# Optimization experiments

Hardware: AMD Instinct MI355X
Metric: run time of the kernel (lower is better)

## Reference

```python
import jax, jax.numpy as jnp
import numpy as np
from jax import lax

B, DZ, H, U, T, V = 256, 512, 512, 16, 16, 512  # batch, latent, lstm hidden, segments, steps/segment, vocab


def setup_inputs() -> dict:
    key = jax.random.key(0)
    ks = jax.random.split(key, 32)
    w = lambda k, shape: jax.random.normal(k, shape, jnp.float32) * 0.05
    d = {
        'z': jax.random.normal(ks[0], (B, DZ), jnp.float32),
        'x': jax.random.randint(ks[1], (B, U * T), 0, V),
        # conductor init-state projection: DZ -> 4H
        'Wc': w(ks[2], (4 * H, DZ)), 'bc': jnp.zeros((4 * H,), jnp.float32),
        # conductor 2-layer LSTM (input H, hidden H)
        'cWih0': w(ks[3], (4 * H, H)), 'cWhh0': w(ks[4], (4 * H, H)),
        'cbih0': jnp.zeros((4 * H,), jnp.float32), 'cbhh0': jnp.zeros((4 * H,), jnp.float32),
        'cWih1': w(ks[5], (4 * H, H)), 'cWhh1': w(ks[6], (4 * H, H)),
        'cbih1': jnp.zeros((4 * H,), jnp.float32), 'cbhh1': jnp.zeros((4 * H,), jnp.float32),
        # decoder init-state projection: H -> 4H
        'Wd': w(ks[7], (4 * H, H)), 'bd': jnp.zeros((4 * H,), jnp.float32),
        # decoder 2-layer LSTM (layer0 input 2H, layer1 input H, hidden H)
        'dWih0': w(ks[8], (4 * H, 2 * H)), 'dWhh0': w(ks[9], (4 * H, H)),
        'dbih0': jnp.zeros((4 * H,), jnp.float32), 'dbhh0': jnp.zeros((4 * H,), jnp.float32),
        'dWih1': w(ks[10], (4 * H, H)), 'dWhh1': w(ks[11], (4 * H, H)),
        'dbih1': jnp.zeros((4 * H,), jnp.float32), 'dbhh1': jnp.zeros((4 * H,), jnp.float32),
        # token embedding and output distribution head
        'emb': w(ks[12], (V, H)),
        'Wo': w(ks[13], (V, H)), 'bo': jnp.zeros((V,), jnp.float32),
    }
    return d


def _cell(x, h, c, Wih, Whh, bih, bhh):
    # PyTorch LSTM gate order: i, f, g, o
    g = x @ Wih.T + bih + h @ Whh.T + bhh
    i, f, gg, o = jnp.split(g, 4, axis=-1)
    c = jax.nn.sigmoid(f) * c + jax.nn.sigmoid(i) * jnp.tanh(gg)
    h = jax.nn.sigmoid(o) * jnp.tanh(c)
    return h, c


def _lstm_layer(xp, h0, c0, Whh, bhh):
    # xp: [N, T, 4H] = precomputed x @ Wih.T + bih
    def step(carry, xg):
        h, c = carry
        g = xg + h @ Whh.T + bhh
        i, f, gg, o = jnp.split(g, 4, axis=-1)
        c = jax.nn.sigmoid(f) * c + jax.nn.sigmoid(i) * jnp.tanh(gg)
        h = jax.nn.sigmoid(o) * jnp.tanh(c)
        return (h, c), h
    _, ys = lax.scan(step, (h0, c0), jnp.swapaxes(xp, 0, 1))
    return jnp.swapaxes(ys, 0, 1)  # [N, T, H]


def reference(z, x, Wc, bc, cWih0, cWhh0, cbih0, cbhh0, cWih1, cWhh1, cbih1, cbhh1,
              Wd, bd, dWih0, dWhh0, dbih0, dbhh0, dWih1, dWhh1, dbih1, dbhh1,
              emb, Wo, bo):
    Bz = z.shape[0]
    # --- conductor ---
    ci = jnp.tanh(z @ Wc.T + bc)  # [B, 4H]
    h1, h2, c1, c2 = ci[:, :H], ci[:, H:2 * H], ci[:, 2 * H:3 * H], ci[:, 3 * H:]
    o0 = jnp.zeros((Bz, H), ci.dtype)

    def cstep(carry, _):
        o, h1, c1, h2, c2 = carry
        h1, c1 = _cell(o, h1, c1, cWih0, cWhh0, cbih0, cbhh0)
        h2, c2 = _cell(h1, h2, c2, cWih1, cWhh1, cbih1, cbhh1)
        return (h2, h1, c1, h2, c2), h2

    _, couts = lax.scan(cstep, (o0, h1, c1, h2, c2), None, length=U)
    cond_out = jnp.swapaxes(couts, 0, 1)  # [B, U, H]

    # --- decoder init states ---
    states = jnp.tanh(cond_out @ Wd.T + bd).reshape(Bz * U, 4 * H)
    dh1, dh2, dc1, dc2 = (states[:, :H], states[:, H:2 * H],
                          states[:, 2 * H:3 * H], states[:, 3 * H:])
    h_init = dh1 + dh2  # [BU, H]

    # --- teacher-forced decoder ---
    xt = x.reshape(Bz * U, T)
    e = emb[xt]  # [BU, T, H]
    e = jnp.concatenate([jnp.zeros((Bz * U, 1, H), e.dtype), e[:, :-1]], axis=1)
    inp = jnp.concatenate(
        [e, jnp.broadcast_to(h_init[:, None], (Bz * U, T, H))], axis=-1)  # [BU, T, 2H]

    y0 = _lstm_layer(inp @ dWih0.T + dbih0, dh1, dc1, dWhh0, dbhh0)
    y1 = _lstm_layer(y0 @ dWih1.T + dbih1, dh2, dc2, dWhh1, dbhh1)
    dist = jax.nn.softmax(y1 @ Wo.T + bo, axis=-1)  # [BU, T, V]
    return dist.reshape(Bz, U * T, V)
```

## Files before the change

kernel.cpp:

```cpp
#include <hip/hip_runtime.h>
#include <math.h>

#define AS1 __attribute__((address_space(1)))
#define AS3 __attribute__((address_space(3)))

typedef __attribute__((ext_vector_type(8))) short short8v;
typedef __attribute__((ext_vector_type(16))) float f32x16;

constexpr size_t PA4c = (size_t)4096 * 512;
constexpr size_t PABc = (size_t)256 * 512;

__device__ __forceinline__ float sigmoidf_(float x) { return 1.f / (1.f + expf(-x)); }
__device__ __forceinline__ unsigned int f2bfu(float f) {
    unsigned int u = __float_as_uint(f);
    return (u + 0x7FFF + ((u >> 16) & 1)) >> 16;
}
__device__ __forceinline__ float bf2f(unsigned int s) { return __uint_as_float(s << 16); }
__device__ __forceinline__ unsigned int pack2(float v) {
    unsigned int b0 = f2bfu(v);
    unsigned int b1 = f2bfu(v - bf2f(b0));
    return b0 | (b1 << 16);
}
__device__ __forceinline__ float unpack2(unsigned int p) { return bf2f(p & 0xffffu) + bf2f(p >> 16); }

__device__ __forceinline__ void xswz(int d, int ngx, int ngy, int& bx, int& by) {
    int nwg = ngx * ngy;
    int q = nwg >> 3, r = nwg & 7, xcd = d & 7, pos = d >> 3;
    int logical = (xcd < r ? xcd * (q + 1) : r * (q + 1) + (xcd - r) * q) + pos;
    bx = logical % ngx; by = logical / ngx;
}

__device__ __forceinline__ size_t offf(int m, int k) {
    return ((size_t)((m >> 5) * 64 + (k >> 3))) * 256 + (size_t)((m & 31) * 8 + (k & 7));
}

__device__ __forceinline__ void store2_coh(unsigned short* p, unsigned int v) {
    asm volatile("global_store_short %0, %1, off sc0 sc1" :: "v"(p), "v"(v) : "memory");
}

template<int N>
__device__ __forceinline__ void wait_vm() {
    asm volatile("s_waitcnt vmcnt(%0) lgkmcnt(0)" :: "n"(N) : "memory");
}

template<int FM, int FN, int NBUF, bool COHB>
__device__ __forceinline__ void gemm_core(
    const short* __restrict__ A1, const short* __restrict__ B1,
    const short* __restrict__ A2, const short* __restrict__ B2,
    int M, int N, int nsteps, int pairSwitch,
    int bx, int by, short* lds, f32x16 (&acc)[FM][FN])
{
    constexpr int ABLK = 4 * FM, BBLK = 2 * FN;
    constexpr int ACH = 2 * ABLK * 2, BCH = 2 * BBLK * 2;
    constexpr int CHT = ACH + BCH;
    constexpr int CPW = CHT / 8;
    constexpr int BUFSH = CHT * 512;
    const int tid = threadIdx.x, lane = tid & 63, wid = tid >> 6;
    const int wm = wid >> 1, wn = wid & 1;
    const int l31 = lane & 31, loct = lane >> 5;
    const int mblk0 = by * ABLK, nblk0 = bx * BBLK;
    const size_t planeA = (size_t)M * 512, planeB = (size_t)N * 512;

    const short* cur[CPW];
    const short* nxt[CPW];
    int ldo[CPW];
    bool isB[CPW];
    #pragma unroll
    for (int i = 0; i < CPW; ++i) {
        int c = wid * CPW + i;
        ldo[i] = c * 512;
        size_t off;
        const short *b1, *b2;
        if (c < ACH) {
            int plane = c / (ABLK * 2), rem = c % (ABLK * 2), blk = rem >> 1, piece = rem & 1;
            off = (size_t)plane * planeA + (size_t)(mblk0 + blk) * 16384 + piece * 512 + lane * 8;
            b1 = A1; b2 = A2; isB[i] = false;
        } else {
            int cb = c - ACH;
            int plane = cb / (BBLK * 2), rem = cb % (BBLK * 2), blk = rem >> 1, piece = rem & 1;
            off = (size_t)plane * planeB + (size_t)(nblk0 + blk) * 16384 + piece * 512 + lane * 8;
            b1 = B1; b2 = B2; isB[i] = true;
        }
        cur[i] = b1 + off;
        nxt[i] = b2 ? (b2 + off) : (b1 + off);
    }

    #pragma unroll
    for (int fm = 0; fm < FM; ++fm)
        #pragma unroll
        for (int fn = 0; fn < FN; ++fn)
            acc[fm][fn] = (f32x16){};

    auto STAGE = [&](int bufIdx) {
        short* db = lds + bufIdx * BUFSH;
        #pragma unroll
        for (int i = 0; i < CPW; ++i) {
            if constexpr (COHB) {
                if (isB[i])
                    __builtin_amdgcn_global_load_lds((const AS1 unsigned int*)cur[i],
                                                     (AS3 unsigned int*)(db + ldo[i]), 16, 0, 17);
                else
                    __builtin_amdgcn_global_load_lds((const AS1 unsigned int*)cur[i],
                                                     (AS3 unsigned int*)(db + ldo[i]), 16, 0, 0);
            } else {
                __builtin_amdgcn_global_load_lds((const AS1 unsigned int*)cur[i],
                                                 (AS3 unsigned int*)(db + ldo[i]), 16, 0, 0);
            }
            cur[i] += 1024;
        }
    };

    #pragma unroll
    for (int i = 0; i < NBUF - 1; ++i) STAGE(i);
    wait_vm<CPW * (NBUF - 2)>();
    __builtin_amdgcn_s_barrier();

    for (int t = 0; t < nsteps; ++t) {
        int s = t + NBUF - 1;
        if (s < nsteps) {
            if (s == pairSwitch) {
                #pragma unroll
                for (int i = 0; i < CPW; ++i) cur[i] = nxt[i];
            }
            STAGE(s % NBUF);
        }
        const short* L = lds + (t % NBUF) * BUFSH;
        #pragma unroll
        for (int ksub = 0; ksub < 2; ++ksub) {
            short8v a[FM][2], b[FN][2];
            #pragma unroll
            for (int p = 0; p < 2; ++p) {
                #pragma unroll
                for (int f = 0; f < FM; ++f)
                    a[f][p] = *(const short8v*)(L + (p * (ABLK * 2) + (wm * FM + f) * 2 + ksub) * 512
                                                  + loct * 256 + l31 * 8);
                #pragma unroll
                for (int f = 0; f < FN; ++f)
                    b[f][p] = *(const short8v*)(L + (ACH + p * (BBLK * 2) + (wn * FN + f) * 2 + ksub) * 512
                                                  + loct * 256 + l31 * 8);
            }
            #pragma unroll
            for (int pp = 0; pp < 3; ++pp) {
                const int pa = (pp == 2) ? 1 : 0, pb = (pp == 1) ? 1 : 0;
                #pragma unroll
                for (int fm = 0; fm < FM; ++fm)
                    #pragma unroll
                    for (int fn = 0; fn < FN; ++fn)
                        acc[fm][fn] = __builtin_amdgcn_mfma_f32_32x32x16_bf16(
                            a[fm][pa], b[fn][pb], acc[fm][fn], 0, 0, 0);
            }
        }
        int ahead = nsteps - 2 - t;
        if (ahead >= NBUF - 2)      wait_vm<CPW * (NBUF - 2)>();
        else if (ahead == 3)        wait_vm<CPW * 3>();
        else if (ahead == 2)        wait_vm<CPW * 2>();
        else if (ahead == 1)        wait_vm<CPW * 1>();
        else                        wait_vm<0>();
        __builtin_amdgcn_s_barrier();
    }
}

template<int FM, int FN>
__device__ __forceinline__ void epi_f32(f32x16 (&acc)[FM][FN], int bx, int by, int N,
                                        float* __restrict__ Cout, const float* __restrict__ bias, int act)
{
    constexpr int ROWS = 128 * FM, COLS = 64 * FN;
    const int tid = threadIdx.x, lane = tid & 63, wid = tid >> 6;
    const int wm = wid >> 1, wn = wid & 1, l31 = lane & 31, loct = lane >> 5;
    #pragma unroll
    for (int fm = 0; fm < FM; ++fm)
        #pragma unroll
        for (int fn = 0; fn < FN; ++fn) {
            int col = bx * COLS + wn * FN * 32 + fn * 32 + l31;
            int rb  = by * ROWS + wm * FM * 32 + fm * 32 + 4 * loct;
            #pragma unroll
            for (int reg = 0; reg < 16; ++reg) {
                int row = rb + (reg & 3) + 8 * (reg >> 2);
                float xv = acc[fm][fn][reg] + (bias ? bias[row] : 0.f);
                if (act) xv = tanhf(xv);
                Cout[(size_t)row * N + col] = xv;
            }
        }
}

template<int FM, int FN>
__device__ __forceinline__ void epi_pack(f32x16 (&acc)[FM][FN], int bx, int by, int N,
                                         unsigned int* __restrict__ packOut)
{
    constexpr int ROWS = 128 * FM, COLS = 64 * FN;
    const int tid = threadIdx.x, lane = tid & 63, wid = tid >> 6;
    const int wm = wid >> 1, wn = wid & 1, l31 = lane & 31, loct = lane >> 5;
    uint4* P4 = (uint4*)packOut;
    #pragma unroll
    for (int fm = 0; fm < FM; ++fm)
        #pragma unroll
        for (int fn = 0; fn < FN; ++fn) {
            int col = bx * COLS + wn * FN * 32 + fn * 32 + l31;
            int ub = by * (ROWS / 4) + wm * FM * 8 + fm * 8 + loct;
            #pragma unroll
            for (int ug = 0; ug < 4; ++ug) {
                int u = ub + 2 * ug;
                uint4 v;
                v.x = pack2(acc[fm][fn][4 * ug + 0]);
                v.y = pack2(acc[fm][fn][4 * ug + 1]);
                v.z = pack2(acc[fm][fn][4 * ug + 2]);
                v.w = pack2(acc[fm][fn][4 * ug + 3]);
                P4[(size_t)u * N + col] = v;
            }
        }
}

template<int FM, int FN>
__device__ __forceinline__ void epi_gate2(
    f32x16 (&acc)[FM][FN], int bx, int by, int N, short* hl,
    const float* __restrict__ bab,
    const unsigned int* __restrict__ hgP,
    const unsigned int* __restrict__ embT,
    const int* __restrict__ xidx,
    float* __restrict__ cT,
    short* __restrict__ hout, size_t hps)
{
    constexpr int ABLK = 4 * FM, BBLK = 2 * FN;
    constexpr int ROWS = 32 * ABLK, COLS = 32 * BBLK;
    constexpr int CHN = ABLK * BBLK * 256;
    const int tid = threadIdx.x, lane = tid & 63, wid = tid >> 6;
    const int wm = wid >> 1, wn = wid & 1, l31 = lane & 31, loct = lane >> 5;
    #pragma unroll
    for (int fm = 0; fm < FM; ++fm) {
        #pragma unroll
        for (int fn = 0; fn < FN; ++fn) {
            const int col = bx * COLS + wn * FN * 32 + fn * 32 + l31;
            const int ub = by * (ROWS / 4) + wm * FM * 8 + fm * 8 + loct;
            int tok = -1;
            if (xidx) tok = xidx[(size_t)col * 16];
            uint4 hv[4]; uint4 ev[4]; float cv[4]; float4 bv[4];
            #pragma unroll
            for (int ug = 0; ug < 4; ++ug) {
                int u = ub + 2 * ug;
                bv[ug] = *(const float4*)&bab[4 * u];
                cv[ug] = cT[(size_t)u * N + col];
                if (hgP) hv[ug] = ((const uint4*)hgP)[(size_t)u * N + col];
            }
            if (embT && tok >= 0) {
                #pragma unroll
                for (int ug = 0; ug < 4; ++ug) {
                    int u = ub + 2 * ug;
                    ev[ug] = ((const uint4*)embT)[(size_t)u * 512 + tok];
                }
            }
            #pragma unroll
            for (int ug = 0; ug < 4; ++ug) {
                int u = ub + 2 * ug;
                float gi = acc[fm][fn][4 * ug + 0] + bv[ug].x;
                float gf = acc[fm][fn][4 * ug + 1] + bv[ug].y;
                float gg = acc[fm][fn][4 * ug + 2] + bv[ug].z;
                float go = acc[fm][fn][4 * ug + 3] + bv[ug].w;
                if (hgP) {
                    gi += unpack2(hv[ug].x); gf += unpack2(hv[ug].y);
                    gg += unpack2(hv[ug].z); go += unpack2(hv[ug].w);
                }
                if (embT && tok >= 0) {
                    gi += unpack2(ev[ug].x); gf += unpack2(ev[ug].y);
                    gg += unpack2(ev[ug].z); go += unpack2(ev[ug].w);
                }
                float c = sigmoidf_(gf) * cv[ug] + sigmoidf_(gi) * tanhf(gg);
                cT[(size_t)u * N + col] = c;
                float h = sigmoidf_(go) * tanhf(c);
                unsigned int p01 = pack2(h);
                int u_loc = wm * FM * 8 + fm * 8 + loct + 2 * ug;
                int m_loc = wn * FN * 32 + fn * 32 + l31;
                int offl = ((m_loc >> 5) * ABLK + (u_loc >> 3)) * 256 + (m_loc & 31) * 8 + (u_loc & 7);
                hl[offl] = (short)(p01 & 0xffffu);
                hl[CHN + offl] = (short)(p01 >> 16);
            }
        }
    }
    __syncthreads();
    constexpr int LB = (ABLK == 8) ? 3 : 2;
    for (int p = 0; p < 2; ++p) {
        for (int jj = tid; jj < CHN / 8; jj += 512) {
            int lc = jj >> 5, m31 = jj & 31;
            int m5 = lc >> LB, u3 = lc & (ABLK - 1);
            size_t gc = (size_t)((bx * BBLK + m5) * 64 + by * ABLK + u3);
            *(short8v*)(hout + p * hps + gc * 256 + m31 * 8) = *(const short8v*)(hl + p * CHN + jj * 8);
        }
    }
}

__device__ __forceinline__ void devbar2(unsigned int* cnt, unsigned int target)
{
    asm volatile("s_waitcnt vmcnt(0)" ::: "memory");
    __syncthreads();
    if (threadIdx.x == 0) {
        __hip_atomic_fetch_add(cnt, 1u, __ATOMIC_RELAXED, __HIP_MEMORY_SCOPE_AGENT);
        int budget = 1 << 22;
        while (__hip_atomic_load(cnt, __ATOMIC_RELAXED, __HIP_MEMORY_SCOPE_AGENT) < target && --budget)
            __builtin_amdgcn_s_sleep(1);
    }
    __syncthreads();
}

template<int FM, int FN>
__global__ __launch_bounds__(512, 1) void gemm_packk(
    const short* A1, const short* B1, const short* A2, const short* B2,
    int M, int N, int nsteps, int psw, unsigned int* packOut)
{
    __shared__ __align__(16) short lds[3 * (2 * (4 * FM) * 2 + 2 * (2 * FN) * 2) * 512];
    int d = blockIdx.y * gridDim.x + blockIdx.x;
    int bx, by; xswz(d, gridDim.x, gridDim.y, bx, by);
    f32x16 acc[FM][FN];
    gemm_core<FM, FN, 3, false>(A1, B1, A2, B2, M, N, nsteps, psw, bx, by, lds, acc);
    epi_pack<FM, FN>(acc, bx, by, N, packOut);
}

template<int FM, int FN>
__global__ __launch_bounds__(512, 1) void gemm_split(
    const short* A1, const short* B1, int M, int N, int nsteps,
    const float* bias, short* hA, short* hB, size_t ps, float* cA, float* cB)
{
    __shared__ __align__(16) short lds[3 * (2 * (4 * FM) * 2 + 2 * (2 * FN) * 2) * 512];
    int d = blockIdx.y * gridDim.x + blockIdx.x;
    int bx, by; xswz(d, gridDim.x, gridDim.y, bx, by);
    f32x16 acc[FM][FN];
    gemm_core<FM, FN, 3, false>(A1, B1, nullptr, nullptr, M, N, nsteps, 100, bx, by, lds, acc);
    constexpr int ROWS = 128 * FM, COLS = 64 * FN;
    const int tid = threadIdx.x, lane = tid & 63, wid = tid >> 6;
    const int wm = wid >> 1, wn = wid & 1, l31 = lane & 31, loct = lane >> 5;
    #pragma unroll
    for (int fm = 0; fm < FM; ++fm)
        #pragma unroll
        for (int fn = 0; fn < FN; ++fn) {
            int col = bx * COLS + wn * FN * 32 + fn * 32 + l31;
            int rb  = by * ROWS + wm * FM * 32 + fm * 32 + 4 * loct;
            #pragma unroll
            for (int reg = 0; reg < 16; ++reg) {
                int row = rb + (reg & 3) + 8 * (reg >> 2);
                float xv = tanhf(acc[fm][fn][reg] + bias[row]);
                if (row < 1024) {
                    short* hp = (row < 512) ? hA : hB;
                    size_t o = offf(col, row & 511);
                    unsigned int p01 = pack2(xv);
                    hp[o] = (short)(p01 & 0xffffu);
                    hp[ps + o] = (short)(p01 >> 16);
                } else {
                    float* cp = (row < 1536) ? cA : cB;
                    cp[(size_t)(row & 511) * N + col] = xv;
                }
            }
        }
}

__global__ __launch_bounds__(512, 1) void cond_lstm(
    const short* cWih0P, const short* cWhh0P, const short* cWih1P, const short* cWhh1P,
    const float* babc0, const float* babc1,
    const float* c1T0, const float* c2T0,
    short* h1p0, short* h1p1, short* h2p0, short* h2p1,
    short* condp, unsigned int* bar)
{
    __shared__ __align__(16) short lds[6 * 24 * 512];
    const int d = blockIdx.x;
    const int xcd = d & 7, slot = d >> 3;
    const int by = xcd * 2 + (slot & 1);
    const int bx = slot >> 1;
    const int tid = threadIdx.x, lane = tid & 63, wid = tid >> 6;
    const int wm = wid >> 1, wn = wid & 1, l31 = lane & 31, loct = lane >> 5;
    const int col = bx * 64 + wn * 32 + l31;
    const int ub = by * 32 + wm * 8 + loct;

    float c1r[4], c2r[4];
    #pragma unroll
    for (int ug = 0; ug < 4; ++ug) {
        int u = ub + 2 * ug;
        c1r[ug] = c1T0[(size_t)u * 256 + col];
        c2r[ug] = c2T0[(size_t)u * 256 + col];
    }

    unsigned int gen = 0;
    for (int s = 0; s < 16; ++s) {
        const int pin = s & 1;
        const short* h1in = pin ? h1p1 : h1p0;  short* h1out = pin ? h1p0 : h1p1;
        const short* h2in = pin ? h2p1 : h2p0;  short* h2out = pin ? h2p0 : h2p1;

        {
            f32x16 acc[1][1];
            if (s == 0)
                gemm_core<1, 1, 6, true>(cWhh0P, h1in, nullptr, nullptr, 2048, 256, 16, 100, bx, by, lds, acc);
            else
                gemm_core<1, 1, 6, true>(cWih0P, h2in, cWhh0P, h1in, 2048, 256, 32, 16, bx, by, lds, acc);
            #pragma unroll
            for (int ug = 0; ug < 4; ++ug) {
                int u = ub + 2 * ug;
                float4 bv = *(const float4*)&babc0[4 * u];
                float gi = acc[0][0][4 * ug + 0] + bv.x;
                float gf = acc[0][0][4 * ug + 1] + bv.y;
                float gg = acc[0][0][4 * ug + 2] + bv.z;
                float go = acc[0][0][4 * ug + 3] + bv.w;
                c1r[ug] = sigmoidf_(gf) * c1r[ug] + sigmoidf_(gi) * tanhf(gg);
                float h = sigmoidf_(go) * tanhf(c1r[ug]);
                unsigned int p01 = pack2(h);
                size_t o = offf(col, u);
                store2_coh((unsigned short*)(h1out + o), p01 & 0xffffu);
                store2_coh((unsigned short*)(h1out + PABc + o), p01 >> 16);
            }
        }
        devbar2(bar, (++gen) * 64);
        {
            f32x16 acc[1][1];
            gemm_core<1, 1, 6, true>(cWih1P, h1out, cWhh1P, h2in, 2048, 256, 32, 16, bx, by, lds, acc);
            #pragma unroll
            for (int ug = 0; ug < 4; ++ug) {
                int u = ub + 2 * ug;
                float4 bv = *(const float4*)&babc1[4 * u];
                float gi = acc[0][0][4 * ug + 0] + bv.x;
                float gf = acc[0][0][4 * ug + 1] + bv.y;
                float gg = acc[0][0][4 * ug + 2] + bv.z;
                float go = acc[0][0][4 * ug + 3] + bv.w;
                c2r[ug] = sigmoidf_(gf) * c2r[ug] + sigmoidf_(gi) * tanhf(gg);
                float h = sigmoidf_(go) * tanhf(c2r[ug]);
                unsigned int p01 = pack2(h);
                size_t o = offf(col, u);
                store2_coh((unsigned short*)(h2out + o), p01 & 0xffffu);
                store2_coh((unsigned short*)(h2out + PABc + o), p01 >> 16);
                int np = col * 16 + s;
                size_t oc = offf(np, u);
                condp[oc] = (short)(p01 & 0xffffu);
                condp[PA4c + oc] = (short)(p01 >> 16);
            }
        }
        devbar2(bar, (++gen) * 64);
    }
}

struct DecArgs {
    const short *dWhh0P, *dWih1P, *dWhh1P, *WoP;
    const float *babd0, *babd1, *bo;
    const unsigned int *hgP, *embT;
    const int* x;
    float *c0T, *c1dT;
    short *h0a, *h0b, *h1da, *h1db;
    float *LgA, *LgB;
    float* out;
    int t;
};

__global__ __launch_bounds__(512, 1) void dec_step(DecArgs A)
{
    __shared__ __align__(16) short lds[3 * 48 * 512];
    const int role = blockIdx.x >> 8;
    const int dd = blockIdx.x & 255;
    const int t = A.t;
    short* h0[2]  = { A.h0a, A.h0b };
    short* h1d[2] = { A.h1da, A.h1db };
    float* Lg[2]  = { A.LgA, A.LgB };

    if (role == 0) {
        if (t <= 15) {
            int pin = t & 1;
            int bx, by; xswz(dd, 32, 8, bx, by);
            f32x16 acc[2][2];
            gemm_core<2, 2, 3, false>(A.dWhh0P, h0[pin], nullptr, nullptr, 2048, 4096, 16, 100, bx, by, lds, acc);
            epi_gate2<2, 2>(acc, bx, by, 4096, lds, A.babd0, A.hgP,
                            t > 0 ? A.embT : nullptr, t > 0 ? A.x + (t - 1) : nullptr,
                            A.c0T, h0[pin ^ 1], PA4c);
            __syncthreads();
        }
        if (t >= 2 && t <= 17) {
            int k = t - 2;
            int bx, by; xswz(dd, 64, 4, bx, by);
            f32x16 acc1[1][1];
            gemm_core<1, 1, 3, false>(A.WoP, h1d[(k + 1) & 1], nullptr, nullptr, 512, 4096, 16, 100, bx, by, lds, acc1);
            epi_f32<1, 1>(acc1, bx, by, 4096, Lg[k & 1], nullptr, 0);
        }
    } else {
        if (t >= 1 && t <= 16) {
            int s = t - 1;
            int pin2 = s & 1;
            int bx, by; xswz(dd, 32, 8, bx, by);
            f32x16 acc[2][2];
            gemm_core<2, 2, 3, false>(A.dWih1P, h0[(s + 1) & 1], A.dWhh1P, h1d[pin2],
                                      2048, 4096, 32, 16, bx, by, lds, acc);
            epi_gate2<2, 2>(acc, bx, by, 4096, lds, A.babd1, nullptr, nullptr, nullptr,
                            A.c1dT, h1d[pin2 ^ 1], PA4c);
            __syncthreads();
        }
        if (t >= 3) {
            int k = t - 3;
            const float* Lsrc = Lg[k & 1];
            float* tile = (float*)lds;
            float* red  = (float*)lds + 16 * 513;
            float* red2 = red + 512;
            const int tid = threadIdx.x;
            const int mj = tid & 15, vs = tid >> 4;
            const int m = dd * 16 + mj;
            float lv[16];
            #pragma unroll
            for (int i = 0; i < 16; ++i) {
                int v = vs * 16 + i;
                lv[i] = Lsrc[(size_t)v * 4096 + m] + A.bo[v];
            }
            float mx = lv[0];
            #pragma unroll
            for (int i = 1; i < 16; ++i) mx = fmaxf(mx, lv[i]);
            red[vs * 16 + mj] = mx;
            __syncthreads();
            for (int o = 16; o >= 1; o >>= 1) {
                if (vs < o) red[vs * 16 + mj] = fmaxf(red[vs * 16 + mj], red[(vs + o) * 16 + mj]);
                __syncthreads();
            }
            mx = red[mj];
            float sum = 0.f;
            #pragma unroll
            for (int i = 0; i < 16; ++i) {
                float e = expf(lv[i] - mx);
                sum += e;
                tile[mj * 513 + vs * 16 + i] = e;
            }
            red2[vs * 16 + mj] = sum;
            __syncthreads();
            for (int o = 16; o >= 1; o >>= 1) {
                if (vs < o) red2[vs * 16 + mj] += red2[(vs + o) * 16 + mj];
                __syncthreads();
            }
            const int r = tid >> 5, c = tid & 31;
            float invr = 1.f / red2[r];
            for (int kk = 0; kk < 16; ++kk) {
                int v = kk * 32 + c;
                A.out[((size_t)(dd * 16 + r) * 16 + k) * 512 + v] = tile[r * 513 + v] * invr;
            }
        }
    }
}

struct PrepEnt { const float* src; const float* src2; void* dst; int ldw, col0, perm, total, op; };
struct PrepArgs { PrepEnt e[18]; int n; };

__global__ void prep_all(PrepArgs pa)
{
    for (int ei = 0; ei < pa.n; ++ei) {
        PrepEnt E = pa.e[ei];
        for (int o = blockIdx.x * 256 + threadIdx.x; o < E.total; o += gridDim.x * 256) {
            if (E.op == 0) {
                int c = o >> 8, w = o & 255, r = w >> 3, jj = w & 7;
                int n = (c >> 6) * 32 + r, k = (c & 63) * 8 + jj;
                int nsrc = E.perm ? ((n >> 2) + 512 * (n & 3)) : n;
                float v = E.src[(size_t)nsrc * E.ldw + E.col0 + k];
                unsigned int b0 = f2bfu(v);
                short* pl = (short*)E.dst;
                pl[o] = (short)b0;
                pl[E.total + o] = (short)f2bfu(v - bf2f(b0));
            } else {
                int src = (o >> 2) + 512 * (o & 3);
                ((float*)E.dst)[o] = E.src[src] + E.src2[src];
            }
        }
    }
}

extern "C" void kernel_launch(void* const* d_in, const int* in_sizes, int n_in,
                              void* d_out, int out_size, void* d_ws, size_t ws_size,
                              hipStream_t stream)
{
    const float* z     = (const float*)d_in[0];
    const int*   x     = (const int*)  d_in[1];
    const float* Wc    = (const float*)d_in[2];
    const float* bc    = (const float*)d_in[3];
    const float* cWih0 = (const float*)d_in[4];
    const float* cWhh0 = (const float*)d_in[5];
    const float* cbih0 = (const float*)d_in[6];
    const float* cbhh0 = (const float*)d_in[7];
    const float* cWih1 = (const float*)d_in[8];
    const float* cWhh1 = (const float*)d_in[9];
    const float* cbih1 = (const float*)d_in[10];
    const float* cbhh1 = (const float*)d_in[11];
    const float* Wd    = (const float*)d_in[12];
    const float* bd    = (const float*)d_in[13];
    const float* dWih0 = (const float*)d_in[14];
    const float* dWhh0 = (const float*)d_in[15];
    const float* dbih0 = (const float*)d_in[16];
    const float* dbhh0 = (const float*)d_in[17];
    const float* dWih1 = (const float*)d_in[18];
    const float* dWhh1 = (const float*)d_in[19];
    const float* dbih1 = (const float*)d_in[20];
    const float* dbhh1 = (const float*)d_in[21];
    const float* emb   = (const float*)d_in[22];
    const float* Wo    = (const float*)d_in[23];
    const float* bo    = (const float*)d_in[24];
    float* out = (float*)d_out;
    (void)in_sizes; (void)n_in; (void)out_size; (void)ws_size;

    char* wsb = (char*)d_ws;
    size_t off = 0;
    auto alloc = [&](size_t bytes) -> void* {
        off = (off + 255) & ~(size_t)255;
        void* p = wsb + off;
        off += bytes;
        return p;
    };
    const size_t PW  = (size_t)2048 * 512;
    const size_t PWo = (size_t)512 * 512;

    short* WcP    = (short*)alloc(2 * PW * 2);
    short* WdP    = (short*)alloc(2 * PW * 2);
    short* dW1P   = (short*)alloc(2 * PW * 2);
    short* dW2P   = (short*)alloc(2 * PW * 2);
    short* cWih0P = (short*)alloc(2 * PW * 2);
    short* cWhh0P = (short*)alloc(2 * PW * 2);
    short* cWih1P = (short*)alloc(2 * PW * 2);
    short* cWhh1P = (short*)alloc(2 * PW * 2);
    short* dWhh0P = (short*)alloc(2 * PW * 2);
    short* dWih1P = (short*)alloc(2 * PW * 2);
    short* dWhh1P = (short*)alloc(2 * PW * 2);
    short* WoP    = (short*)alloc(2 * PWo * 2);
    short* zpl    = (short*)alloc(2 * PABc * 2);
    short* embpl  = (short*)alloc(2 * PWo * 2);
    float* babc0  = (float*)alloc(2048 * 4);
    float* babc1  = (float*)alloc(2048 * 4);
    float* babd0  = (float*)alloc(2048 * 4);
    float* babd1  = (float*)alloc(2048 * 4);
    float* GbufT  = (float*)alloc((size_t)2048 * 4096 * 4);
    unsigned int* hinitgP = (unsigned int*)alloc((size_t)512 * 4096 * 4 * 4);
    unsigned int* embW0P  = (unsigned int*)alloc((size_t)512 * 512 * 4 * 4);
    short* h1pl0 = (short*)alloc(2 * PABc * 2);
    short* h1pl1 = (short*)alloc(2 * PABc * 2);
    short* h2pl0 = (short*)alloc(2 * PABc * 2);
    short* h2pl1 = (short*)alloc(2 * PABc * 2);
    float* c1T = (float*)alloc((size_t)512 * 256 * 4);
    float* c2T = (float*)alloc((size_t)512 * 256 * 4);
    short* condpl = (short*)alloc(2 * PA4c * 2);
    short* h0pl[2];  short* h1dpl[2];
    h0pl[0]  = (short*)alloc(2 * PA4c * 2); h0pl[1]  = (short*)alloc(2 * PA4c * 2);
    h1dpl[0] = (short*)alloc(2 * PA4c * 2); h1dpl[1] = (short*)alloc(2 * PA4c * 2);
    float* c0T  = (float*)alloc((size_t)512 * 4096 * 4);
    float* c1dT = (float*)alloc((size_t)512 * 4096 * 4);
    unsigned int* barreg = (unsigned int*)alloc(512);

    float* Lg[2] = { GbufT, GbufT + (size_t)512 * 4096 };

    PrepArgs pa; pa.n = 18;
    auto W8 = [](const float* s, void* d, int ldw, int col0, int perm, int total) {
        PrepEnt e; e.src = s; e.src2 = nullptr; e.dst = d; e.ldw = ldw; e.col0 = col0;
        e.perm = perm; e.total = total; e.op = 0; return e;
    };
    auto B8 = [](const float* a, const float* b, void* d) {
        PrepEnt e; e.src = a; e.src2 = b; e.dst = d; e.ldw = 0; e.col0 = 0;
        e.perm = 0; e.total = 2048; e.op = 1; return e;
    };
    pa.e[0]  = W8(Wc,    WcP,    512,  0,   0, 2048 * 512);
    pa.e[1]  = W8(Wd,    WdP,    512,  0,   0, 2048 * 512);
    pa.e[2]  = W8(dWih0, dW1P,   1024, 0,   1, 2048 * 512);
    pa.e[3]  = W8(dWih0, dW2P,   1024, 512, 1, 2048 * 512);
    pa.e[4]  = W8(cWih0, cWih0P, 512,  0,   1, 2048 * 512);
    pa.e[5]  = W8(cWhh0, cWhh0P, 512,  0,   1, 2048 * 512);
    pa.e[6]  = W8(cWih1, cWih1P, 512,  0,   1, 2048 * 512);
    pa.e[7]  = W8(cWhh1, cWhh1P, 512,  0,   1, 2048 * 512);
    pa.e[8]  = W8(dWhh0, dWhh0P, 512,  0,   1, 2048 * 512);
    pa.e[9]  = W8(dWih1, dWih1P, 512,  0,   1, 2048 * 512);
    pa.e[10] = W8(dWhh1, dWhh1P, 512,  0,   1, 2048 * 512);
    pa.e[11] = W8(Wo,    WoP,    512,  0,   0, 512 * 512);
    pa.e[12] = W8(z,     zpl,    512,  0,   0, 256 * 512);
    pa.e[13] = W8(emb,   embpl,  512,  0,   0, 512 * 512);
    pa.e[14] = B8(cbih0, cbhh0, babc0);
    pa.e[15] = B8(cbih1, cbhh1, babc1);
    pa.e[16] = B8(dbih0, dbhh0, babd0);
    pa.e[17] = B8(dbih1, dbhh1, babd1);
    prep_all<<<dim3(1024), dim3(256), 0, stream>>>(pa);
    hipMemsetAsync(barreg, 0, 512, stream);

    gemm_split<2, 2><<<dim3(2, 8), dim3(512), 0, stream>>>(
        WcP, zpl, 2048, 256, 16, bc, h1pl0, h2pl0, PABc, c1T, c2T);

    gemm_packk<2, 2><<<dim3(4, 8), dim3(512), 0, stream>>>(
        dW1P, embpl, nullptr, nullptr, 2048, 512, 16, 100, embW0P);

    cond_lstm<<<dim3(64), dim3(512), 0, stream>>>(
        cWih0P, cWhh0P, cWih1P, cWhh1P, babc0, babc1, c1T, c2T,
        h1pl0, h1pl1, h2pl0, h2pl1, condpl, barreg);

    gemm_split<2, 2><<<dim3(32, 8), dim3(512), 0, stream>>>(
        WdP, condpl, 2048, 4096, 16, bd, h0pl[0], h1dpl[0], PA4c, c0T, c1dT);

    gemm_packk<2, 2><<<dim3(32, 8), dim3(512), 0, stream>>>(
        dW2P, h0pl[0], dW2P, h1dpl[0], 2048, 4096, 32, 16, hinitgP);

    for (int t = 0; t <= 18; ++t) {
        DecArgs A;
        A.dWhh0P = dWhh0P; A.dWih1P = dWih1P; A.dWhh1P = dWhh1P; A.WoP = WoP;
        A.babd0 = babd0; A.babd1 = babd1; A.bo = bo;
        A.hgP = hinitgP; A.embT = embW0P; A.x = x;
        A.c0T = c0T; A.c1dT = c1dT;
        A.h0a = h0pl[0]; A.h0b = h0pl[1]; A.h1da = h1dpl[0]; A.h1db = h1dpl[1];
        A.LgA = Lg[0]; A.LgB = Lg[1];
        A.out = out; A.t = t;
        dec_step<<<dim3(512), dim3(512), 0, stream>>>(A);
    }
}
```

Baseline: 2.493 ms.

## Split conductor LSTM across more blocks with LDS-resident hidden-state tiles

The persistent conductor LSTM kernel goes from 64 blocks of 512 threads to 128 blocks of 256 threads, with each block owning a narrower 32-column slice. Each block loads its whole recurrent-input (B) slice into LDS once per cell via direct global-to-LDS loads. It then streams weight (A) tiles through a 3-deep LDS ring buffer, replacing the generic gemm_core with a hand-written bf16x2 split MFMA loop. The intent is to use more CUs for the latency-bound recurrence and overlap weight loads with compute. The cost is a per-k-step block barrier and a device-wide barrier spanning twice as many blocks.

```diff
diff --git a/kernel.cpp b/kernel.cpp
--- a/kernel.cpp
+++ b/kernel.cpp
@@ -350,22 +350,26 @@
         }
 }
 
-__global__ __launch_bounds__(512, 1) void cond_lstm(
+__global__ __launch_bounds__(256, 1) void cond_lstm(
     const short* cWih0P, const short* cWhh0P, const short* cWih1P, const short* cWhh1P,
     const float* babc0, const float* babc1,
     const float* c1T0, const float* c2T0,
     short* h1p0, short* h1p1, short* h2p0, short* h2p1,
     short* condp, unsigned int* bar)
 {
-    __shared__ __align__(16) short lds[6 * 24 * 512];
+    __shared__ __align__(16) short Blds[2][2][16384];
+    __shared__ __align__(16) short Alds[3][4096];
+
     const int d = blockIdx.x;
     const int xcd = d & 7, slot = d >> 3;
     const int by = xcd * 2 + (slot & 1);
     const int bx = slot >> 1;
-    const int tid = threadIdx.x, lane = tid & 63, wid = tid >> 6;
-    const int wm = wid >> 1, wn = wid & 1, l31 = lane & 31, loct = lane >> 5;
-    const int col = bx * 64 + wn * 32 + l31;
-    const int ub = by * 32 + wm * 8 + loct;
+    const int tid = threadIdx.x;
+    const int lane = tid & 63, wid = tid >> 6;
+    const int l31 = lane & 31, loct = lane >> 5;
+    const int mblk0 = by * 4;
+    const int col = bx * 32 + l31;
+    const int ub = by * 32 + wid * 8 + loct;
 
     float c1r[4], c2r[4];
     #pragma unroll
@@ -381,53 +385,82 @@
         const short* h1in = pin ? h1p1 : h1p0;  short* h1out = pin ? h1p0 : h1p1;
         const short* h2in = pin ? h2p1 : h2p0;  short* h2out = pin ? h2p0 : h2p1;
 
-        {
-            f32x16 acc[1][1];
-            if (s == 0)
-                gemm_core<1, 1, 6, true>(cWhh0P, h1in, nullptr, nullptr, 2048, 256, 16, 100, bx, by, lds, acc);
-            else
-                gemm_core<1, 1, 6, true>(cWih0P, h2in, cWhh0P, h1in, 2048, 256, 32, 16, bx, by, lds, acc);
+        for (int cell = 0; cell < 2; ++cell) {
+            const short* Am[2]; const short* Bm[2]; int nmat;
+            if (cell == 0) {
+                if (s == 0) { Am[0] = cWhh0P; Bm[0] = h1in; Am[1] = cWhh0P; Bm[1] = h1in; nmat = 1; }
+                else        { Am[0] = cWih0P; Bm[0] = h2in; Am[1] = cWhh0P; Bm[1] = h1in; nmat = 2; }
+            } else {
+                Am[0] = cWih1P; Bm[0] = h1out; Am[1] = cWhh1P; Bm[1] = h2in; nmat = 2;
+            }
+            for (int m = 0; m < nmat; ++m) {
+                #pragma unroll
+                for (int i = 0; i < 16; ++i) {
+                    int q = tid + i * 256;
+                    int pl = q >> 11, r = q & 2047;
+                    __builtin_amdgcn_global_load_lds(
+                        (const AS1 unsigned int*)(Bm[m] + (size_t)pl * PABc + bx * 16384 + r * 8),
+                        (AS3 unsigned int*)(&Blds[m][pl][r * 8]), 16, 0, 17);
+                }
+            }
+            const int T = nmat * 32;
+            auto stageA = [&](int t) {
+                const short* Ab = Am[t >> 5];
+                int tk = t & 31;
+                #pragma unroll
+                for (int i = 0; i < 2; ++i) {
+                    int q = tid + i * 256;
+                    int pl = q >> 8, blk = (q >> 6) & 3, kp = (q >> 5) & 1, lp = q & 31;
+                    __builtin_amdgcn_global_load_lds(
+                        (const AS1 unsigned int*)(Ab + (size_t)pl * ((size_t)2048 * 512)
+                                                  + (size_t)(mblk0 + blk) * 16384 + (tk * 2 + kp) * 256 + lp * 8),
+                        (AS3 unsigned int*)(&Alds[t % 3][q * 8]), 16, 0, 0);
+                }
+            };
+            stageA(0); stageA(1);
+            wait_vm<2>();
+            __builtin_amdgcn_s_barrier();
+            f32x16 acc = {};
+            for (int t = 0; t < T; ++t) {
+                if (t + 2 < T) stageA(t + 2);
+                const short* Ab = &Alds[t % 3][0];
+                int mt = t >> 5, tk = t & 31;
+                short8v ah = *(const short8v*)(Ab + wid * 512 + loct * 256 + l31 * 8);
+                short8v al = *(const short8v*)(Ab + 2048 + wid * 512 + loct * 256 + l31 * 8);
+                short8v bh = *(const short8v*)(&Blds[mt][0][(tk * 2 + loct) * 256 + l31 * 8]);
+                short8v bl = *(const short8v*)(&Blds[mt][1][(tk * 2 + loct) * 256 + l31 * 8]);
+                acc = __builtin_amdgcn_mfma_f32_32x32x16_bf16(ah, bh, acc, 0, 0, 0);
+                acc = __builtin_amdgcn_mfma_f32_32x32x16_bf16(ah, bl, acc, 0, 0, 0);
+                acc = __builtin_amdgcn_mfma_f32_32x32x16_bf16(al, bh, acc, 0, 0, 0);
+                if (t + 2 < T) wait_vm<2>(); else wait_vm<0>();
+                __builtin_amdgcn_s_barrier();
+            }
+            const float* bab = cell ? babc1 : babc0;
+            float* cr = cell ? c2r : c1r;
+            short* hdst = cell ? h2out : h1out;
             #pragma unroll
             for (int ug = 0; ug < 4; ++ug) {
                 int u = ub + 2 * ug;
-                float4 bv = *(const float4*)&babc0[4 * u];
-                float gi = acc[0][0][4 * ug + 0] + bv.x;
-                float gf = acc[0][0][4 * ug + 1] + bv.y;
-                float gg = acc[0][0][4 * ug + 2] + bv.z;
-                float go = acc[0][0][4 * ug + 3] + bv.w;
-                c1r[ug] = sigmoidf_(gf) * c1r[ug] + sigmoidf_(gi) * tanhf(gg);
-                float h = sigmoidf_(go) * tanhf(c1r[ug]);
+                float4 bv = *(const float4*)&bab[4 * u];
+                float gi = acc[4 * ug + 0] + bv.x;
+                float gf = acc[4 * ug + 1] + bv.y;
+                float gg = acc[4 * ug + 2] + bv.z;
+                float go = acc[4 * ug + 3] + bv.w;
+                cr[ug] = sigmoidf_(gf) * cr[ug] + sigmoidf_(gi) * tanhf(gg);
+                float h = sigmoidf_(go) * tanhf(cr[ug]);
                 unsigned int p01 = pack2(h);
                 size_t o = offf(col, u);
-                store2_coh((unsigned short*)(h1out + o), p01 & 0xffffu);
-                store2_coh((unsigned short*)(h1out + PABc + o), p01 >> 16);
-            }
-        }
-        devbar2(bar, (++gen) * 64);
-        {
-            f32x16 acc[1][1];
-            gemm_core<1, 1, 6, true>(cWih1P, h1out, cWhh1P, h2in, 2048, 256, 32, 16, bx, by, lds, acc);
-            #pragma unroll
-            for (int ug = 0; ug < 4; ++ug) {
-                int u = ub + 2 * ug;
-                float4 bv = *(const float4*)&babc1[4 * u];
-                float gi = acc[0][0][4 * ug + 0] + bv.x;
-                float gf = acc[0][0][4 * ug + 1] + bv.y;
-                float gg = acc[0][0][4 * ug + 2] + bv.z;
-                float go = acc[0][0][4 * ug + 3] + bv.w;
-                c2r[ug] = sigmoidf_(gf) * c2r[ug] + sigmoidf_(gi) * tanhf(gg);
-                float h = sigmoidf_(go) * tanhf(c2r[ug]);
-                unsigned int p01 = pack2(h);
-                size_t o = offf(col, u);
-                store2_coh((unsigned short*)(h2out + o), p01 & 0xffffu);
-                store2_coh((unsigned short*)(h2out + PABc + o), p01 >> 16);
-                int np = col * 16 + s;
-                size_t oc = offf(np, u);
-                condp[oc] = (short)(p01 & 0xffffu);
-                condp[PA4c + oc] = (short)(p01 >> 16);
-            }
-        }
-        devbar2(bar, (++gen) * 64);
+                store2_coh((unsigned short*)(hdst + o), p01 & 0xffffu);
+                store2_coh((unsigned short*)(hdst + PABc + o), p01 >> 16);
+                if (cell == 1) {
+                    int np = col * 16 + s;
+                    size_t oc = offf(np, u);
+                    condp[oc] = (short)(p01 & 0xffffu);
+                    condp[PA4c + oc] = (short)(p01 >> 16);
+                }
+            }
+            devbar2(bar, (++gen) * 128);
+        }
     }
 }
 
@@ -672,7 +705,7 @@
     gemm_packk<2, 2><<<dim3(4, 8), dim3(512), 0, stream>>>(
         dW1P, embpl, nullptr, nullptr, 2048, 512, 16, 100, embW0P);
 
-    cond_lstm<<<dim3(64), dim3(512), 0, stream>>>(
+    cond_lstm<<<dim3(128), dim3(256), 0, stream>>>(
         cWih0P, cWhh0P, cWih1P, cWhh1P, babc0, babc1, c1T, c2T,
         h1pl0, h1pl1, h2pl0, h2pl1, condpl, barreg);
 
```

After: 3.084 ms. 23.7% more time.

## Replace persistent conductor kernel with per-cell launches instead of device barriers

Applied to the files above, without the earlier changes.

The persistent conductor LSTM kernel, which synchronised 64 blocks through atomic spin barriers and coherent stores, is replaced by 32 separate cell kernel launches, each running the shared GEMM core and the gate epilogue. The conductor output write moves into the gate epilogue. The GEMM core loses its buffer-depth and coherence template parameters and is fixed at triple buffering. This removes the spin-barrier and coherent-store overhead but adds kernel launch latency and loses the deeper 6-stage pipeline for the small conductor GEMMs.

```diff
diff --git a/kernel.cpp b/kernel.cpp
--- a/kernel.cpp
+++ b/kernel.cpp
@@ -34,16 +34,12 @@
     return ((size_t)((m >> 5) * 64 + (k >> 3))) * 256 + (size_t)((m & 31) * 8 + (k & 7));
 }
 
-__device__ __forceinline__ void store2_coh(unsigned short* p, unsigned int v) {
-    asm volatile("global_store_short %0, %1, off sc0 sc1" :: "v"(p), "v"(v) : "memory");
-}
-
 template<int N>
 __device__ __forceinline__ void wait_vm() {
     asm volatile("s_waitcnt vmcnt(%0) lgkmcnt(0)" :: "n"(N) : "memory");
 }
 
-template<int FM, int FN, int NBUF, bool COHB>
+template<int FM, int FN>
 __device__ __forceinline__ void gemm_core(
     const short* __restrict__ A1, const short* __restrict__ B1,
     const short* __restrict__ A2, const short* __restrict__ B2,
@@ -54,6 +50,7 @@
     constexpr int ACH = 2 * ABLK * 2, BCH = 2 * BBLK * 2;
     constexpr int CHT = ACH + BCH;
     constexpr int CPW = CHT / 8;
+    constexpr int NBUF = 3;
     constexpr int BUFSH = CHT * 512;
     const int tid = threadIdx.x, lane = tid & 63, wid = tid >> 6;
     const int wm = wid >> 1, wn = wid & 1;
@@ -64,7 +61,6 @@
     const short* cur[CPW];
     const short* nxt[CPW];
     int ldo[CPW];
-    bool isB[CPW];
     #pragma unroll
     for (int i = 0; i < CPW; ++i) {
         int c = wid * CPW + i;
@@ -74,12 +70,12 @@
         if (c < ACH) {
             int plane = c / (ABLK * 2), rem = c % (ABLK * 2), blk = rem >> 1, piece = rem & 1;
             off = (size_t)plane * planeA + (size_t)(mblk0 + blk) * 16384 + piece * 512 + lane * 8;
-            b1 = A1; b2 = A2; isB[i] = false;
+            b1 = A1; b2 = A2;
         } else {
             int cb = c - ACH;
             int plane = cb / (BBLK * 2), rem = cb % (BBLK * 2), blk = rem >> 1, piece = rem & 1;
             off = (size_t)plane * planeB + (size_t)(nblk0 + blk) * 16384 + piece * 512 + lane * 8;
-            b1 = B1; b2 = B2; isB[i] = true;
+            b1 = B1; b2 = B2;
         }
         cur[i] = b1 + off;
         nxt[i] = b2 ? (b2 + off) : (b1 + off);
@@ -95,24 +91,14 @@
         short* db = lds + bufIdx * BUFSH;
         #pragma unroll
         for (int i = 0; i < CPW; ++i) {
-            if constexpr (COHB) {
-                if (isB[i])
-                    __builtin_amdgcn_global_load_lds((const AS1 unsigned int*)cur[i],
-                                                     (AS3 unsigned int*)(db + ldo[i]), 16, 0, 17);
-                else
-                    __builtin_amdgcn_global_load_lds((const AS1 unsigned int*)cur[i],
-                                                     (AS3 unsigned int*)(db + ldo[i]), 16, 0, 0);
-            } else {
-                __builtin_amdgcn_global_load_lds((const AS1 unsigned int*)cur[i],
-                                                 (AS3 unsigned int*)(db + ldo[i]), 16, 0, 0);
-            }
+            __builtin_amdgcn_global_load_lds((const AS1 unsigned int*)cur[i],
+                                             (AS3 unsigned int*)(db + ldo[i]), 16, 0, 0);
             cur[i] += 1024;
         }
     };
 
-    #pragma unroll
-    for (int i = 0; i < NBUF - 1; ++i) STAGE(i);
-    wait_vm<CPW * (NBUF - 2)>();
+    STAGE(0); STAGE(1);
+    wait_vm<CPW>();
     __builtin_amdgcn_s_barrier();
 
     for (int t = 0; t < nsteps; ++t) {
@@ -150,12 +136,8 @@
                             a[fm][pa], b[fn][pb], acc[fm][fn], 0, 0, 0);
             }
         }
-        int ahead = nsteps - 2 - t;
-        if (ahead >= NBUF - 2)      wait_vm<CPW * (NBUF - 2)>();
-        else if (ahead == 3)        wait_vm<CPW * 3>();
-        else if (ahead == 2)        wait_vm<CPW * 2>();
-        else if (ahead == 1)        wait_vm<CPW * 1>();
-        else                        wait_vm<0>();
+        if (t + 2 < nsteps) wait_vm<CPW>();
+        else                wait_vm<0>();
         __builtin_amdgcn_s_barrier();
     }
 }
@@ -218,7 +200,8 @@
     const unsigned int* __restrict__ embT,
     const int* __restrict__ xidx,
     float* __restrict__ cT,
-    short* __restrict__ hout, size_t hps)
+    short* __restrict__ hout, size_t hps,
+    short* __restrict__ condp, int ustep)
 {
     constexpr int ABLK = 4 * FM, BBLK = 2 * FN;
     constexpr int ROWS = 32 * ABLK, COLS = 32 * BBLK;
@@ -272,6 +255,12 @@
                 int offl = ((m_loc >> 5) * ABLK + (u_loc >> 3)) * 256 + (m_loc & 31) * 8 + (u_loc & 7);
                 hl[offl] = (short)(p01 & 0xffffu);
                 hl[CHN + offl] = (short)(p01 >> 16);
+                if (condp) {
+                    int np = col * 16 + ustep;
+                    size_t oc = offf(np, u);
+                    condp[oc] = (short)(p01 & 0xffffu);
+                    condp[PA4c + oc] = (short)(p01 >> 16);
+                }
             }
         }
     }
@@ -287,19 +276,6 @@
     }
 }
 
-__device__ __forceinline__ void devbar2(unsigned int* cnt, unsigned int target)
-{
-    asm volatile("s_waitcnt vmcnt(0)" ::: "memory");
-    __syncthreads();
-    if (threadIdx.x == 0) {
-        __hip_atomic_fetch_add(cnt, 1u, __ATOMIC_RELAXED, __HIP_MEMORY_SCOPE_AGENT);
-        int budget = 1 << 22;
-        while (__hip_atomic_load(cnt, __ATOMIC_RELAXED, __HIP_MEMORY_SCOPE_AGENT) < target && --budget)
-            __builtin_amdgcn_s_sleep(1);
-    }
-    __syncthreads();
-}
-
 template<int FM, int FN>
 __global__ __launch_bounds__(512, 1) void gemm_packk(
     const short* A1, const short* B1, const short* A2, const short* B2,
@@ -309,7 +285,7 @@
     int d = blockIdx.y * gridDim.x + blockIdx.x;
     int bx, by; xswz(d, gridDim.x, gridDim.y, bx, by);
     f32x16 acc[FM][FN];
-    gemm_core<FM, FN, 3, false>(A1, B1, A2, B2, M, N, nsteps, psw, bx, by, lds, acc);
+    gemm_core<FM, FN>(A1, B1, A2, B2, M, N, nsteps, psw, bx, by, lds, acc);
     epi_pack<FM, FN>(acc, bx, by, N, packOut);
 }
 
@@ -322,7 +298,7 @@
     int d = blockIdx.y * gridDim.x + blockIdx.x;
     int bx, by; xswz(d, gridDim.x, gridDim.y, bx, by);
     f32x16 acc[FM][FN];
-    gemm_core<FM, FN, 3, false>(A1, B1, nullptr, nullptr, M, N, nsteps, 100, bx, by, lds, acc);
+    gemm_core<FM, FN>(A1, B1, nullptr, nullptr, M, N, nsteps, 100, bx, by, lds, acc);
     constexpr int ROWS = 128 * FM, COLS = 64 * FN;
     const int tid = threadIdx.x, lane = tid & 63, wid = tid >> 6;
     const int wm = wid >> 1, wn = wid & 1, l31 = lane & 31, loct = lane >> 5;
@@ -350,85 +326,19 @@
         }
 }
 
-__global__ __launch_bounds__(512, 1) void cond_lstm(
-    const short* cWih0P, const short* cWhh0P, const short* cWih1P, const short* cWhh1P,
-    const float* babc0, const float* babc1,
-    const float* c1T0, const float* c2T0,
-    short* h1p0, short* h1p1, short* h2p0, short* h2p1,
-    short* condp, unsigned int* bar)
-{
-    __shared__ __align__(16) short lds[6 * 24 * 512];
-    const int d = blockIdx.x;
-    const int xcd = d & 7, slot = d >> 3;
-    const int by = xcd * 2 + (slot & 1);
-    const int bx = slot >> 1;
-    const int tid = threadIdx.x, lane = tid & 63, wid = tid >> 6;
-    const int wm = wid >> 1, wn = wid & 1, l31 = lane & 31, loct = lane >> 5;
-    const int col = bx * 64 + wn * 32 + l31;
-    const int ub = by * 32 + wm * 8 + loct;
-
-    float c1r[4], c2r[4];
-    #pragma unroll
-    for (int ug = 0; ug < 4; ++ug) {
-        int u = ub + 2 * ug;
-        c1r[ug] = c1T0[(size_t)u * 256 + col];
-        c2r[ug] = c2T0[(size_t)u * 256 + col];
-    }
-
-    unsigned int gen = 0;
-    for (int s = 0; s < 16; ++s) {
-        const int pin = s & 1;
-        const short* h1in = pin ? h1p1 : h1p0;  short* h1out = pin ? h1p0 : h1p1;
-        const short* h2in = pin ? h2p1 : h2p0;  short* h2out = pin ? h2p0 : h2p1;
-
-        {
-            f32x16 acc[1][1];
-            if (s == 0)
-                gemm_core<1, 1, 6, true>(cWhh0P, h1in, nullptr, nullptr, 2048, 256, 16, 100, bx, by, lds, acc);
-            else
-                gemm_core<1, 1, 6, true>(cWih0P, h2in, cWhh0P, h1in, 2048, 256, 32, 16, bx, by, lds, acc);
-            #pragma unroll
-            for (int ug = 0; ug < 4; ++ug) {
-                int u = ub + 2 * ug;
-                float4 bv = *(const float4*)&babc0[4 * u];
-                float gi = acc[0][0][4 * ug + 0] + bv.x;
-                float gf = acc[0][0][4 * ug + 1] + bv.y;
-                float gg = acc[0][0][4 * ug + 2] + bv.z;
-                float go = acc[0][0][4 * ug + 3] + bv.w;
-                c1r[ug] = sigmoidf_(gf) * c1r[ug] + sigmoidf_(gi) * tanhf(gg);
-                float h = sigmoidf_(go) * tanhf(c1r[ug]);
-                unsigned int p01 = pack2(h);
-                size_t o = offf(col, u);
-                store2_coh((unsigned short*)(h1out + o), p01 & 0xffffu);
-                store2_coh((unsigned short*)(h1out + PABc + o), p01 >> 16);
-            }
-        }
-        devbar2(bar, (++gen) * 64);
-        {
-            f32x16 acc[1][1];
-            gemm_core<1, 1, 6, true>(cWih1P, h1out, cWhh1P, h2in, 2048, 256, 32, 16, bx, by, lds, acc);
-            #pragma unroll
-            for (int ug = 0; ug < 4; ++ug) {
-                int u = ub + 2 * ug;
-                float4 bv = *(const float4*)&babc1[4 * u];
-                float gi = acc[0][0][4 * ug + 0] + bv.x;
-                float gf = acc[0][0][4 * ug + 1] + bv.y;
-                float gg = acc[0][0][4 * ug + 2] + bv.z;
-                float go = acc[0][0][4 * ug + 3] + bv.w;
-                c2r[ug] = sigmoidf_(gf) * c2r[ug] + sigmoidf_(gi) * tanhf(gg);
-                float h = sigmoidf_(go) * tanhf(c2r[ug]);
-                unsigned int p01 = pack2(h);
-                size_t o = offf(col, u);
-                store2_coh((unsigned short*)(h2out + o), p01 & 0xffffu);
-                store2_coh((unsigned short*)(h2out + PABc + o), p01 >> 16);
-                int np = col * 16 + s;
-                size_t oc = offf(np, u);
-                condp[oc] = (short)(p01 & 0xffffu);
-                condp[PA4c + oc] = (short)(p01 >> 16);
-            }
-        }
-        devbar2(bar, (++gen) * 64);
-    }
+__global__ __launch_bounds__(512, 1) void cond_cell(
+    const short* A1, const short* B1, const short* A2, const short* B2,
+    int nsteps, int psw,
+    const float* bab, float* cT,
+    short* hout, short* condp, int ustep)
+{
+    __shared__ __align__(16) short lds[3 * 24 * 512];
+    int d = blockIdx.y * gridDim.x + blockIdx.x;
+    int bx, by; xswz(d, gridDim.x, gridDim.y, bx, by);
+    f32x16 acc[1][1];
+    gemm_core<1, 1>(A1, B1, A2, B2, 2048, 256, nsteps, psw, bx, by, lds, acc);
+    epi_gate2<1, 1>(acc, bx, by, 256, lds, bab, nullptr, nullptr, nullptr,
+                    cT, hout, PABc, condp, ustep);
 }
 
 struct DecArgs {
@@ -458,17 +368,17 @@
             int pin = t & 1;
             int bx, by; xswz(dd, 32, 8, bx, by);
             f32x16 acc[2][2];
-            gemm_core<2, 2, 3, false>(A.dWhh0P, h0[pin], nullptr, nullptr, 2048, 4096, 16, 100, bx, by, lds, acc);
+            gemm_core<2, 2>(A.dWhh0P, h0[pin], nullptr, nullptr, 2048, 4096, 16, 100, bx, by, lds, acc);
             epi_gate2<2, 2>(acc, bx, by, 4096, lds, A.babd0, A.hgP,
                             t > 0 ? A.embT : nullptr, t > 0 ? A.x + (t - 1) : nullptr,
-                            A.c0T, h0[pin ^ 1], PA4c);
+                            A.c0T, h0[pin ^ 1], PA4c, nullptr, 0);
             __syncthreads();
         }
         if (t >= 2 && t <= 17) {
             int k = t - 2;
             int bx, by; xswz(dd, 64, 4, bx, by);
             f32x16 acc1[1][1];
-            gemm_core<1, 1, 3, false>(A.WoP, h1d[(k + 1) & 1], nullptr, nullptr, 512, 4096, 16, 100, bx, by, lds, acc1);
+            gemm_core<1, 1>(A.WoP, h1d[(k + 1) & 1], nullptr, nullptr, 512, 4096, 16, 100, bx, by, lds, acc1);
             epi_f32<1, 1>(acc1, bx, by, 4096, Lg[k & 1], nullptr, 0);
         }
     } else {
@@ -477,10 +387,10 @@
             int pin2 = s & 1;
             int bx, by; xswz(dd, 32, 8, bx, by);
             f32x16 acc[2][2];
-            gemm_core<2, 2, 3, false>(A.dWih1P, h0[(s + 1) & 1], A.dWhh1P, h1d[pin2],
-                                      2048, 4096, 32, 16, bx, by, lds, acc);
+            gemm_core<2, 2>(A.dWih1P, h0[(s + 1) & 1], A.dWhh1P, h1d[pin2],
+                            2048, 4096, 32, 16, bx, by, lds, acc);
             epi_gate2<2, 2>(acc, bx, by, 4096, lds, A.babd1, nullptr, nullptr, nullptr,
-                            A.c1dT, h1d[pin2 ^ 1], PA4c);
+                            A.c1dT, h1d[pin2 ^ 1], PA4c, nullptr, 0);
             __syncthreads();
         }
         if (t >= 3) {
@@ -620,10 +530,9 @@
     float* GbufT  = (float*)alloc((size_t)2048 * 4096 * 4);
     unsigned int* hinitgP = (unsigned int*)alloc((size_t)512 * 4096 * 4 * 4);
     unsigned int* embW0P  = (unsigned int*)alloc((size_t)512 * 512 * 4 * 4);
-    short* h1pl0 = (short*)alloc(2 * PABc * 2);
-    short* h1pl1 = (short*)alloc(2 * PABc * 2);
-    short* h2pl0 = (short*)alloc(2 * PABc * 2);
-    short* h2pl1 = (short*)alloc(2 * PABc * 2);
+    short* h1pl[2]; short* h2pl[2];
+    h1pl[0] = (short*)alloc(2 * PABc * 2);  h1pl[1] = (short*)alloc(2 * PABc * 2);
+    h2pl[0] = (short*)alloc(2 * PABc * 2);  h2pl[1] = (short*)alloc(2 * PABc * 2);
     float* c1T = (float*)alloc((size_t)512 * 256 * 4);
     float* c2T = (float*)alloc((size_t)512 * 256 * 4);
     short* condpl = (short*)alloc(2 * PA4c * 2);
@@ -632,7 +541,6 @@
     h1dpl[0] = (short*)alloc(2 * PA4c * 2); h1dpl[1] = (short*)alloc(2 * PA4c * 2);
     float* c0T  = (float*)alloc((size_t)512 * 4096 * 4);
     float* c1dT = (float*)alloc((size_t)512 * 4096 * 4);
-    unsigned int* barreg = (unsigned int*)alloc(512);
 
     float* Lg[2] = { GbufT, GbufT + (size_t)512 * 4096 };
 
@@ -664,17 +572,27 @@
     pa.e[16] = B8(dbih0, dbhh0, babd0);
     pa.e[17] = B8(dbih1, dbhh1, babd1);
     prep_all<<<dim3(1024), dim3(256), 0, stream>>>(pa);
-    hipMemsetAsync(barreg, 0, 512, stream);
 
     gemm_split<2, 2><<<dim3(2, 8), dim3(512), 0, stream>>>(
-        WcP, zpl, 2048, 256, 16, bc, h1pl0, h2pl0, PABc, c1T, c2T);
+        WcP, zpl, 2048, 256, 16, bc, h1pl[0], h2pl[0], PABc, c1T, c2T);
 
     gemm_packk<2, 2><<<dim3(4, 8), dim3(512), 0, stream>>>(
         dW1P, embpl, nullptr, nullptr, 2048, 512, 16, 100, embW0P);
 
-    cond_lstm<<<dim3(64), dim3(512), 0, stream>>>(
-        cWih0P, cWhh0P, cWih1P, cWhh1P, babc0, babc1, c1T, c2T,
-        h1pl0, h1pl1, h2pl0, h2pl1, condpl, barreg);
+    for (int u = 0; u < 16; ++u) {
+        int pin = u & 1;
+        if (u == 0)
+            cond_cell<<<dim3(4, 16), dim3(512), 0, stream>>>(
+                cWhh0P, h1pl[0], nullptr, nullptr, 16, 100,
+                babc0, c1T, h1pl[1], nullptr, 0);
+        else
+            cond_cell<<<dim3(4, 16), dim3(512), 0, stream>>>(
+                cWih0P, h2pl[pin], cWhh0P, h1pl[pin], 32, 16,
+                babc0, c1T, h1pl[pin ^ 1], nullptr, 0);
+        cond_cell<<<dim3(4, 16), dim3(512), 0, stream>>>(
+            cWih1P, h1pl[pin ^ 1], cWhh1P, h2pl[pin], 32, 16,
+            babc1, c2T, h2pl[pin ^ 1], condpl, u);
+    }
 
     gemm_split<2, 2><<<dim3(32, 8), dim3(512), 0, stream>>>(
         WdP, condpl, 2048, 4096, 16, bd, h0pl[0], h1dpl[0], PA4c, c0T, c1dT);
```

Result: faster. 2.402 ms, median of 2 (-3.6%).
